# Optimization experiments

Hardware: AMD Instinct MI355X
Metric: run time of the kernel (lower is better)

Reference implementation:

```python
import jax, jax.numpy as jnp
from jax import lax
import numpy as np

SEQ = 1024
VOCAB = 50000
EMB = 300
CAS_V, CAS_D = 8, 50
POS_V, POS_D = 48, 50
IN_DIM = EMB + CAS_D + POS_D  # 400
H = 512
T = 13  # num_classes / CRF tags


def setup_inputs() -> dict:
    key = jax.random.key(0)
    ks = jax.random.split(key, 16)
    s = lambda k, shape, sc=0.05: jax.random.normal(k, shape, dtype=jnp.float32) * sc
    return {
        "x": jax.random.randint(ks[0], (SEQ,), 0, VOCAB),
        "casing": jax.random.randint(ks[1], (SEQ,), 0, CAS_V),
        "pos": jax.random.randint(ks[2], (SEQ,), 0, POS_V),
        "h0": jnp.zeros((2, H), dtype=jnp.float32),
        "c0": jnp.zeros((2, H), dtype=jnp.float32),
        "W_emb": s(ks[3], (VOCAB, EMB)),
        "W_cas": s(ks[4], (CAS_V, CAS_D)),
        "W_pos": s(ks[5], (POS_V, POS_D)),
        "Wx_f": s(ks[6], (IN_DIM, 4 * H)),
        "Wh_f": s(ks[7], (H, 4 * H)),
        "b_f": jnp.zeros((4 * H,), dtype=jnp.float32),
        "Wx_b": s(ks[8], (IN_DIM, 4 * H)),
        "Wh_b": s(ks[9], (H, 4 * H)),
        "b_b": jnp.zeros((4 * H,), dtype=jnp.float32),
        "W_out": s(ks[10], (2 * H, T)),
        "b_out": jnp.zeros((T,), dtype=jnp.float32),
        "trans": s(ks[11], (T, T), 0.1),
        "start_trans": s(ks[12], (T,), 0.1),
        "end_trans": s(ks[13], (T,), 0.1),
    }


def _lstm_dir(feat, Wx, Wh, b, h0, c0, reverse):
    # feat: [L, IN_DIM]; precompute input projection for all steps
    pre = feat @ Wx + b  # [L, 4H]

    def step(carry, p):
        h, c = carry
        z = p + h @ Wh
        i, f, g, o = jnp.split(z, 4, axis=-1)
        c = jax.nn.sigmoid(f) * c + jax.nn.sigmoid(i) * jnp.tanh(g)
        h = jax.nn.sigmoid(o) * jnp.tanh(c)
        return (h, c), h

    _, hs = lax.scan(step, (h0, c0), pre, reverse=reverse)
    return hs  # [L, H]


def _viterbi(em, trans, start_trans, end_trans):
    # em: [L, T] emission (log) scores; max-plus DP
    score0 = start_trans + em[0]

    def fwd(score, e):
        total = score[:, None] + trans  # [T, T]: prev -> next
        best = jnp.max(total, axis=0) + e
        idx = jnp.argmax(total, axis=0)
        return best, idx

    final, hist = lax.scan(fwd, score0, em[1:])  # hist: [L-1, T]
    final = final + end_trans
    last = jnp.argmax(final)

    def back(tag, idx_row):
        return idx_row[tag], tag

    first, rest = lax.scan(back, last, hist, reverse=True)
    return jnp.concatenate([first[None], rest])  # [L] int


def reference(x, casing, pos, h0, c0, W_emb, W_cas, W_pos, Wx_f, Wh_f, b_f,
              Wx_b, Wh_b, b_b, W_out, b_out, trans, start_trans, end_trans):
    # AWD-LSTM encode (eval mode: dropout identity)
    feat = jnp.concatenate([W_emb[x], W_cas[casing], W_pos[pos]], axis=-1)  # [L, 400]
    hf = _lstm_dir(feat, Wx_f, Wh_f, b_f, h0[0], c0[0], reverse=False)
    hb = _lstm_dir(feat, Wx_b, Wh_b, b_b, h0[1], c0[1], reverse=True)
    o = jnp.concatenate([hf, hb], axis=-1) @ W_out + b_out  # [L, T]
    tag_scores = jax.nn.log_softmax(o, axis=1)
    path = _viterbi(tag_scores, trans, start_trans, end_trans)
    return tag_scores, path
```

## Files before the change

### kernel.cpp

```cpp
#include <hip/hip_runtime.h>
#include <hip/hip_bf16.h>
#include <math.h>

#define SEQ 1024
#define HID 512
#define FOURH 2048
#define IND 400
#define NT 13

#define LSTM_WGS 64
#define NGEMM 192
#define JPW 16
#define WCOLS 64
#define TAG_INVALID 0xFFFFFFFFu

__device__ __forceinline__ float bf2f(unsigned short u) {
    union { unsigned u32; float f; } v;
    v.u32 = ((unsigned)u) << 16;
    return v.f;
}

__device__ __forceinline__ unsigned short f2bf(float f) {
    union { float f; unsigned u; } v;
    v.f = f;
    unsigned u = v.u;
    unsigned rounding = 0x7FFFu + ((u >> 16) & 1u);
    u += rounding;
    return (unsigned short)(u >> 16);
}

__device__ __forceinline__ float ldf(const void* p, size_t i, int isf32) {
    return isf32 ? ((const float*)p)[i] : bf2f(((const unsigned short*)p)[i]);
}

__device__ __forceinline__ float fsigm(float x) {
    return __builtin_amdgcn_rcpf(1.f + __builtin_amdgcn_exp2f(-1.44269504f * x));
}
__device__ __forceinline__ float ftanhf(float x) {
    return 1.f - 2.f * __builtin_amdgcn_rcpf(__builtin_amdgcn_exp2f(2.88539008f * x) + 1.f);
}
__device__ __forceinline__ float satz(float z) { return fminf(fmaxf(z, -60.f), 60.f); }

__global__ __launch_bounds__(64) void detect_kernel(const unsigned short* __restrict__ w,
                                                    int* __restrict__ flag,
                                                    unsigned* __restrict__ vcnt,
                                                    unsigned* __restrict__ flags) {
    int lane = threadIdx.x;
    int cnt = 0;
    for (int i = 0; i < 4; ++i) {
        unsigned short u = w[2 * (lane * 4 + i)];
        int e = (u >> 7) & 0xFF;
        if (e >= 90 && e < 127) cnt++;
    }
#pragma unroll
    for (int off = 32; off >= 1; off >>= 1) cnt += __shfl_xor(cnt, off, 64);
    if (lane == 0) *flag = (cnt < 128) ? 1 : 0;
    if (lane == 1) *vcnt = 0;
    flags[lane] = 0;
}

__global__ __launch_bounds__(512, 2) void fused_kernel(
        const int* __restrict__ x, const int* __restrict__ cas, const int* __restrict__ pos,
        const void* __restrict__ W_emb, const void* __restrict__ W_cas, const void* __restrict__ W_pos,
        const void* __restrict__ Wx_f, const void* __restrict__ b_f,
        const void* __restrict__ Wx_b, const void* __restrict__ b_b,
        const void* __restrict__ Wh_f, const void* __restrict__ Wh_b,
        const void* __restrict__ h0, const void* __restrict__ c0,
        unsigned long long* __restrict__ preu, float* __restrict__ hsout,
        unsigned long long* hbuf, const int* __restrict__ dflag,
        unsigned* __restrict__ flags) {
    __shared__ float smem[12800 + 96];
    const int isf32 = *dflag;
    const int tid = threadIdx.x;
    const int b = blockIdx.x;

    if (b >= LSTM_WGS) {
        const int e = b - LSTM_WGS;
        const int gdir = e & 1;
        const int i = e >> 1;
        const void* Wx = gdir ? Wx_b : Wx_f;
        const void* bb = gdir ? b_b : b_f;
        unsigned long long* dst = preu + (size_t)gdir * SEQ * 512;
        float* ftile = smem;
        int* idxs = (int*)&smem[12800];
        const int critby = gdir ? 31 : 0;

        if (i < 8) {
            const int r0 = critby * 32;
            const int c  = tid & 255;
            const int rg = tid >> 8;
            const int col = i * 256 + c;

            if (tid < 32)       idxs[tid] = x[r0 + tid];
            else if (tid < 64)  idxs[tid] = cas[r0 + tid - 32];
            else if (tid < 96)  idxs[tid] = pos[r0 + tid - 64];
            __syncthreads();
            for (int idx = tid; idx < 32 * IND; idx += 512) {
                int r = idx / IND;
                int el = idx - r * IND;
                float v;
                if (el < 300)      v = ldf(W_emb, (size_t)idxs[r] * 300 + el, isf32);
                else if (el < 350) v = ldf(W_cas, (size_t)idxs[32 + r] * 50 + (el - 300), isf32);
                else               v = ldf(W_pos, (size_t)idxs[64 + r] * 50 + (el - 350), isf32);
                ftile[idx] = v;
            }
            __syncthreads();

            float acc[16];
            float bias = ldf(bb, col, isf32);
#pragma unroll
            for (int r = 0; r < 16; ++r) acc[r] = bias;

            if (isf32) {
                const float* W = (const float*)Wx;
                for (int kk = 0; kk < 100; ++kk) {
                    int k = kk * 4;
                    float w0 = W[(size_t)(k + 0) * FOURH + col];
                    float w1 = W[(size_t)(k + 1) * FOURH + col];
                    float w2 = W[(size_t)(k + 2) * FOURH + col];
                    float w3 = W[(size_t)(k + 3) * FOURH + col];
#pragma unroll
                    for (int rr = 0; rr < 16; ++rr) {
                        float4 f = *(const float4*)&ftile[(rg * 16 + rr) * IND + k];
                        acc[rr] += f.x * w0 + f.y * w1 + f.z * w2 + f.w * w3;
                    }
                }
            } else {
                const unsigned short* W = (const unsigned short*)Wx;
                for (int kk = 0; kk < 100; ++kk) {
                    int k = kk * 4;
                    float w0 = bf2f(W[(size_t)(k + 0) * FOURH + col]);
                    float w1 = bf2f(W[(size_t)(k + 1) * FOURH + col]);
                    float w2 = bf2f(W[(size_t)(k + 2) * FOURH + col]);
                    float w3 = bf2f(W[(size_t)(k + 3) * FOURH + col]);
#pragma unroll
                    for (int rr = 0; rr < 16; ++rr) {
                        float4 f = *(const float4*)&ftile[(rg * 16 + rr) * IND + k];
                        acc[rr] += f.x * w0 + f.y * w1 + f.z * w2 + f.w * w3;
                    }
                }
            }

            for (int rr = 0; rr < 16; ++rr) {
                int r = rg * 16 + rr;
                unsigned long long w = ((unsigned long long)f2bf(acc[rr])) << (16 * (tid & 3));
                w |= __shfl_xor(w, 1, 64);
                w |= __shfl_xor(w, 2, 64);
                if ((tid & 3) == 0)
                    __hip_atomic_store(&dst[(size_t)(r0 + r) * 512 + (col >> 2)], w,
                                       __ATOMIC_RELAXED, __HIP_MEMORY_SCOPE_AGENT);
            }
            asm volatile("s_waitcnt vmcnt(0)" ::: "memory");
            __syncthreads();
            if (tid == 0) atomicAdd(&flags[gdir * 32 + critby], 1u);
            return;
        }

        const int j = i - 8;
        const int q = j >> 2;
        const int ntile = (j < 36) ? 2 : 1;
        for (int ti = 0; ti < ntile; ++ti) {
            const int by = (ti == 0) ? (gdir ? (30 - q) : (1 + q))
                                     : (gdir ? (8 - q)  : (23 + q));
            const int bx = j & 3;
            const int r0 = by * 32;
            const int col = bx * 512 + tid;

            __syncthreads();
            if (tid < 32)       idxs[tid] = x[r0 + tid];
            else if (tid < 64)  idxs[tid] = cas[r0 + tid - 32];
            else if (tid < 96)  idxs[tid] = pos[r0 + tid - 64];
            __syncthreads();
            for (int idx = tid; idx < 32 * IND; idx += 512) {
                int r = idx / IND;
                int el = idx - r * IND;
                float v;
                if (el < 300)      v = ldf(W_emb, (size_t)idxs[r] * 300 + el, isf32);
                else if (el < 350) v = ldf(W_cas, (size_t)idxs[32 + r] * 50 + (el - 300), isf32);
                else               v = ldf(W_pos, (size_t)idxs[64 + r] * 50 + (el - 350), isf32);
                ftile[idx] = v;
            }
            __syncthreads();

            float acc[32];
            float bias = ldf(bb, col, isf32);
#pragma unroll
            for (int r = 0; r < 32; ++r) acc[r] = bias;

            if (isf32) {
                const float* W = (const float*)Wx;
                for (int kk = 0; kk < 100; ++kk) {
                    int k = kk * 4;
                    float w0 = W[(size_t)(k + 0) * FOURH + col];
                    float w1 = W[(size_t)(k + 1) * FOURH + col];
                    float w2 = W[(size_t)(k + 2) * FOURH + col];
                    float w3 = W[(size_t)(k + 3) * FOURH + col];
#pragma unroll
                    for (int r = 0; r < 32; ++r) {
                        float4 f = *(const float4*)&ftile[r * IND + k];
                        acc[r] += f.x * w0 + f.y * w1 + f.z * w2 + f.w * w3;
                    }
                }
            } else {
                const unsigned short* W = (const unsigned short*)Wx;
                for (int kk = 0; kk < 100; ++kk) {
                    int k = kk * 4;
                    float w0 = bf2f(W[(size_t)(k + 0) * FOURH + col]);
                    float w1 = bf2f(W[(size_t)(k + 1) * FOURH + col]);
                    float w2 = bf2f(W[(size_t)(k + 2) * FOURH + col]);
                    float w3 = bf2f(W[(size_t)(k + 3) * FOURH + col]);
#pragma unroll
                    for (int r = 0; r < 32; ++r) {
                        float4 f = *(const float4*)&ftile[r * IND + k];
                        acc[r] += f.x * w0 + f.y * w1 + f.z * w2 + f.w * w3;
                    }
                }
            }

            for (int r = 0; r < 32; ++r) {
                unsigned long long w = ((unsigned long long)f2bf(acc[r])) << (16 * (tid & 3));
                w |= __shfl_xor(w, 1, 64);
                w |= __shfl_xor(w, 2, 64);
                if ((tid & 3) == 0)
                    __hip_atomic_store(&dst[(size_t)(r0 + r) * 512 + (col >> 2)], w,
                                       __ATOMIC_RELAXED, __HIP_MEMORY_SCOPE_AGENT);
            }
            asm volatile("s_waitcnt vmcnt(0)" ::: "memory");
            __syncthreads();
            if (tid == 0) atomicAdd(&flags[gdir * 32 + by], 1u);
        }
        return;
    }

    float* redp = smem;
    const int dir = b & 1;
    const int g = b >> 1;
    const int j0 = g * JPW;
    const int critby = dir ? 31 : 0;

    const void* Wh = dir ? Wh_b : Wh_f;
    const unsigned long long* preu_d = preu + (size_t)dir * SEQ * 512;
    float* hso = hsout + (size_t)dir * SEQ * HID;
    unsigned long long* hb_d  = hbuf + dir * 2 * HID;
    unsigned long long* hb2_d = hbuf + 4096 + dir * 2 * HID;

    const int seg  = tid >> 6;
    const int col  = tid & 63;
    const int unit = col & 15;
    const int gate = col >> 4;
    const int gcol = gate * HID + j0 + unit;
    const int redoff = seg * WCOLS + unit * 4 + gate;

    const int isep  = (tid < 64);
    const int eunit = tid >> 2;
    const int egate = tid & 3;
    const int ispub = isep && (egate == 0);
    const int sub   = eunit & 3;
    const int widx  = egate * 128 + ((j0 + eunit) >> 2);

    float4 w0, w1, w2, w3, w4, w5, w6, w7, w8, w9, w10, w11, w12, w13, w14, w15;
    if (isf32) {
        const float* wp = (const float*)Wh + (size_t)(seg * 64) * FOURH + gcol;
#define LDW(i) w##i = make_float4(wp[(size_t)(4*i+0)*FOURH], wp[(size_t)(4*i+1)*FOURH], \
                                  wp[(size_t)(4*i+2)*FOURH], wp[(size_t)(4*i+3)*FOURH])
        LDW(0); LDW(1); LDW(2); LDW(3); LDW(4); LDW(5); LDW(6); LDW(7);
        LDW(8); LDW(9); LDW(10); LDW(11); LDW(12); LDW(13); LDW(14); LDW(15);
#undef LDW
    } else {
        const unsigned short* wp = (const unsigned short*)Wh + (size_t)(seg * 64) * FOURH + gcol;
#define LDW(i) w##i = make_float4(bf2f(wp[(size_t)(4*i+0)*FOURH]), bf2f(wp[(size_t)(4*i+1)*FOURH]), \
                                  bf2f(wp[(size_t)(4*i+2)*FOURH]), bf2f(wp[(size_t)(4*i+3)*FOURH]))
        LDW(0); LDW(1); LDW(2); LDW(3); LDW(4); LDW(5); LDW(6); LDW(7);
        LDW(8); LDW(9); LDW(10); LDW(11); LDW(12); LDW(13); LDW(14); LDW(15);
#undef LDW
    }

    float creg = 0.f;
    unsigned long long znw = 0;
    int curby = critby;
    if (isep) {
        if (ispub) {
            creg = ldf(c0, dir * HID + j0 + eunit, isf32);
            float h0v = ldf(h0, dir * HID + j0 + eunit, isf32);
            unsigned long long wv = (unsigned long long)__float_as_uint(h0v);
            unsigned long long iv = ((unsigned long long)TAG_INVALID << 32);
            __hip_atomic_store(&hb_d[j0 + eunit],        wv, __ATOMIC_RELAXED, __HIP_MEMORY_SCOPE_AGENT);
            __hip_atomic_store(&hb2_d[j0 + eunit],       wv, __ATOMIC_RELAXED, __HIP_MEMORY_SCOPE_AGENT);
            __hip_atomic_store(&hb_d[HID + j0 + eunit],  iv, __ATOMIC_RELAXED, __HIP_MEMORY_SCOPE_AGENT);
            __hip_atomic_store(&hb2_d[HID + j0 + eunit], iv, __ATOMIC_RELAXED, __HIP_MEMORY_SCOPE_AGENT);
        }
        {
            const unsigned* fp = &flags[dir * 32 + curby];
            while (__hip_atomic_load(fp, __ATOMIC_RELAXED, __HIP_MEMORY_SCOPE_AGENT) < 8u) {}
        }
        int t0 = dir ? (SEQ - 1) : 0;
        znw = __hip_atomic_load(&preu_d[(size_t)t0 * 512 + widx],
                                __ATOMIC_RELAXED, __HIP_MEMORY_SCOPE_AGENT);
    }
    __syncthreads();

    for (int s = 0; s < SEQ; ++s) {
        const int t = dir ? (SEQ - 1 - s) : s;

        unsigned hu;
        {
            const unsigned long long* A = &hb_d[(s & 1) * HID + tid];
            const unsigned long long* B = &hb2_d[(s & 1) * HID + tid];
            const unsigned expect = (unsigned)s;
            unsigned long long va = __hip_atomic_load(A, __ATOMIC_RELAXED, __HIP_MEMORY_SCOPE_AGENT);
            unsigned long long vb = __hip_atomic_load(B, __ATOMIC_RELAXED, __HIP_MEMORY_SCOPE_AGENT);
            for (;;) {
                if ((unsigned)(va >> 32) == expect) { hu = (unsigned)va; break; }
                va = __hip_atomic_load(A, __ATOMIC_RELAXED, __HIP_MEMORY_SCOPE_AGENT);
                if ((unsigned)(vb >> 32) == expect) { hu = (unsigned)vb; break; }
                vb = __hip_atomic_load(B, __ATOMIC_RELAXED, __HIP_MEMORY_SCOPE_AGENT);
            }
        }

        float zc = 0.f;
        if (isep) {
            zc = bf2f((unsigned short)(znw >> (16 * sub)));
            if (s + 1 < SEQ) {
                int tn = dir ? (SEQ - 2 - s) : (s + 1);
                int byn = tn >> 5;
                if (byn != curby) {
                    const unsigned thr = (byn == critby) ? 8u : 4u;
                    const unsigned* fp = &flags[dir * 32 + byn];
                    while (__hip_atomic_load(fp, __ATOMIC_RELAXED, __HIP_MEMORY_SCOPE_AGENT) < thr) {}
                    curby = byn;
                }
                znw = __hip_atomic_load(&preu_d[(size_t)tn * 512 + widx],
                                        __ATOMIC_RELAXED, __HIP_MEMORY_SCOPE_AGENT);
            }
        }

        float a0 = 0.f, a1 = 0.f, a2 = 0.f, a3 = 0.f;
#define MACQ(i, A) { \
        float hx = __uint_as_float((unsigned)__builtin_amdgcn_readlane((int)hu, 4*i+0)); \
        float hy = __uint_as_float((unsigned)__builtin_amdgcn_readlane((int)hu, 4*i+1)); \
        float hz = __uint_as_float((unsigned)__builtin_amdgcn_readlane((int)hu, 4*i+2)); \
        float hw = __uint_as_float((unsigned)__builtin_amdgcn_readlane((int)hu, 4*i+3)); \
        A += hx * w##i.x + hy * w##i.y + hz * w##i.z + hw * w##i.w; }
        MACQ(0, a0)  MACQ(1, a1)  MACQ(2, a2)  MACQ(3, a3)
        MACQ(4, a0)  MACQ(5, a1)  MACQ(6, a2)  MACQ(7, a3)
        MACQ(8, a0)  MACQ(9, a1)  MACQ(10, a2) MACQ(11, a3)
        MACQ(12, a0) MACQ(13, a1) MACQ(14, a2) MACQ(15, a3)
#undef MACQ
        redp[(s & 1) * 512 + redoff] = (a0 + a1) + (a2 + a3);
        __syncthreads();

        if (isep) {
            const float* rp = &redp[(s & 1) * 512];
            float z = rp[0 * WCOLS + tid] + rp[1 * WCOLS + tid]
                    + rp[2 * WCOLS + tid] + rp[3 * WCOLS + tid]
                    + rp[4 * WCOLS + tid] + rp[5 * WCOLS + tid]
                    + rp[6 * WCOLS + tid] + rp[7 * WCOLS + tid];
            z = satz(z + zc);
            float vs = fsigm(z);
            float vt = ftanhf(z);
            float v = (egate == 2) ? vt : vs;
            float x1 = __shfl_xor(v, 1, 64);
            float x2 = __shfl_xor(v, 2, 64);
            float x3 = __shfl_xor(x1, 2, 64);
            if (ispub) {
                float ig = v, fg = x1, gg = x2, og = x3;
                float cnew = fg * creg + ig * gg;
                creg = cnew;
                float hnew = og * ftanhf(satz(cnew));
                unsigned long long w = ((unsigned long long)(unsigned)(s + 1) << 32)
                                     | (unsigned long long)__float_as_uint(hnew);
                const int par = (s + 1) & 1;
                __hip_atomic_store(&hb_d[par * HID + j0 + eunit], w,
                                   __ATOMIC_RELAXED, __HIP_MEMORY_SCOPE_AGENT);
                __hip_atomic_store(&hb2_d[par * HID + j0 + eunit], w,
                                   __ATOMIC_RELAXED, __HIP_MEMORY_SCOPE_AGENT);
                hso[(size_t)t * HID + j0 + eunit] = hnew;
            }
        }
    }
}

__global__ __launch_bounds__(64) void outproj_kernel(const float* __restrict__ hsout,
        const void* __restrict__ W_out, const void* __restrict__ b_out,
        float* __restrict__ out_scores,
        const void* __restrict__ trans, const void* __restrict__ strans,
        const void* __restrict__ etrans, float* __restrict__ out_path,
        unsigned* __restrict__ vcnt, const int* __restrict__ dflag) {
    __shared__ unsigned char hist[SEQ][NT];
    const int isf32 = *dflag;
    int t = blockIdx.x;
    int lane = threadIdx.x;
    const float* hf = hsout + (size_t)t * HID;
    const float* hb = hsout + (size_t)SEQ * HID + (size_t)t * HID;
    float acc[NT];
#pragma unroll
    for (int j = 0; j < NT; ++j) acc[j] = 0.f;
    for (int k = lane; k < HID; k += 64) {
        float a = hf[k], b2 = hb[k];
#pragma unroll
        for (int j = 0; j < NT; ++j)
            acc[j] += a * ldf(W_out, (size_t)k * NT + j, isf32)
                    + b2 * ldf(W_out, (size_t)(HID + k) * NT + j, isf32);
    }
#pragma unroll
    for (int off = 32; off >= 1; off >>= 1) {
#pragma unroll
        for (int j = 0; j < NT; ++j) acc[j] += __shfl_xor(acc[j], off, 64);
    }
    float o[NT];
    float m = -1e30f;
#pragma unroll
    for (int j = 0; j < NT; ++j) { o[j] = acc[j] + ldf(b_out, j, isf32); m = fmaxf(m, o[j]); }
    float lse = 0.f;
#pragma unroll
    for (int j = 0; j < NT; ++j) lse += expf(o[j] - m);
    lse = m + logf(lse);
    if (lane < NT)
        __hip_atomic_store(&out_scores[t * NT + lane], o[lane] - lse,
                           __ATOMIC_RELAXED, __HIP_MEMORY_SCOPE_AGENT);
    __builtin_amdgcn_s_waitcnt(0);

    unsigned old = 0;
    if (lane == 0) old = atomicAdd(vcnt, 1u);
    old = __shfl(old, 0, 64);
    if (old != SEQ - 1) return;

    const float* em = out_scores;
    int j = lane < NT ? lane : 0;
    float tr[NT];
#pragma unroll
    for (int i = 0; i < NT; ++i) tr[i] = ldf(trans, i * NT + j, isf32);
#define EML(tt) __hip_atomic_load(&em[(size_t)(tt) * NT + j], __ATOMIC_RELAXED, __HIP_MEMORY_SCOPE_AGENT)
    float score = ldf(strans, j, isf32) + EML(0);
    float c0 = EML(1), c1 = EML(2), c2 = EML(3), c3 = EML(4),
          c4 = EML(5), c5 = EML(6), c6 = EML(7), c7 = EML(8);
#define VSTEP(PE, TT) { \
    float best = -1e30f; int arg = 0; \
    _Pragma("unroll") \
    for (int i = 0; i < NT; ++i) { \
        float si = __shfl(score, i, 64); \
        float cand = si + tr[i]; \
        if (cand > best) { best = cand; arg = i; } \
    } \
    if (lane < NT) hist[TT][lane] = (unsigned char)arg; \
    score = best + PE; }
    for (int tb = 1; tb < SEQ; tb += 8) {
        int nb = tb + 8;
        float n0 = 0.f, n1 = 0.f, n2 = 0.f, n3 = 0.f, n4 = 0.f, n5 = 0.f, n6 = 0.f, n7 = 0.f;
        if (nb + 0 < SEQ) n0 = EML(nb + 0);
        if (nb + 1 < SEQ) n1 = EML(nb + 1);
        if (nb + 2 < SEQ) n2 = EML(nb + 2);
        if (nb + 3 < SEQ) n3 = EML(nb + 3);
        if (nb + 4 < SEQ) n4 = EML(nb + 4);
        if (nb + 5 < SEQ) n5 = EML(nb + 5);
        if (nb + 6 < SEQ) n6 = EML(nb + 6);
        if (nb + 7 < SEQ) n7 = EML(nb + 7);
        VSTEP(c0, tb + 0)
        if (tb + 1 < SEQ) VSTEP(c1, tb + 1)
        if (tb + 2 < SEQ) VSTEP(c2, tb + 2)
        if (tb + 3 < SEQ) VSTEP(c3, tb + 3)
        if (tb + 4 < SEQ) VSTEP(c4, tb + 4)
        if (tb + 5 < SEQ) VSTEP(c5, tb + 5)
        if (tb + 6 < SEQ) VSTEP(c6, tb + 6)
        if (tb + 7 < SEQ) VSTEP(c7, tb + 7)
        c0 = n0; c1 = n1; c2 = n2; c3 = n3; c4 = n4; c5 = n5; c6 = n6; c7 = n7;
    }
#undef VSTEP
#undef EML
    score += ldf(etrans, j, isf32);
    float bmax = -1e30f;
    int last = 0;
#pragma unroll
    for (int i = 0; i < NT; ++i) {
        float si = __shfl(score, i, 64);
        if (si > bmax) { bmax = si; last = i; }
    }
    if (lane == 0) {
        int cur = last;
        out_path[SEQ - 1] = (float)cur;
        for (int tt = SEQ - 1; tt >= 1; --tt) {
            cur = hist[tt][cur];
            out_path[tt - 1] = (float)cur;
        }
    }
}

extern "C" void kernel_launch(void* const* d_in, const int* in_sizes, int n_in,
                              void* d_out, int out_size, void* d_ws, size_t ws_size,
                              hipStream_t stream) {
    const int* x      = (const int*)d_in[0];
    const int* casing = (const int*)d_in[1];
    const int* posi   = (const int*)d_in[2];
    const void* h0    = d_in[3];
    const void* c0    = d_in[4];
    const void* W_emb = d_in[5];
    const void* W_cas = d_in[6];
    const void* W_pos = d_in[7];
    const void* Wx_f  = d_in[8];
    const void* Wh_f  = d_in[9];
    const void* b_f   = d_in[10];
    const void* Wx_b  = d_in[11];
    const void* Wh_b  = d_in[12];
    const void* b_b   = d_in[13];
    const void* W_out = d_in[14];
    const void* b_out = d_in[15];
    const void* trans = d_in[16];
    const void* strans = d_in[17];
    const void* etrans = d_in[18];

    char* ws = (char*)d_ws;
    int* dflag          = (int*)(ws + 448);
    unsigned* vcnt      = (unsigned*)(ws + 456);
    unsigned long long* preu = (unsigned long long*)(ws + 512);
    float* hsout        = (float*)(ws + 512 + 8388608);
    unsigned long long* hbuf = (unsigned long long*)(ws + 512 + 8388608 + 4194304);
    unsigned* flags     = (unsigned*)(ws + 512 + 8388608 + 4194304 + 65536);

    float* out_scores = (float*)d_out;
    float* out_path   = out_scores + SEQ * NT;

    detect_kernel<<<1, 64, 0, stream>>>((const unsigned short*)W_emb, dflag, vcnt, flags);

    fused_kernel<<<LSTM_WGS + NGEMM, 512, 0, stream>>>(
        x, casing, posi, W_emb, W_cas, W_pos, Wx_f, b_f, Wx_b, b_b,
        Wh_f, Wh_b, h0, c0, preu, hsout, hbuf, dflag, flags);

    outproj_kernel<<<SEQ, 64, 0, stream>>>(hsout, W_out, b_out, out_scores,
                                           trans, strans, etrans, out_path, vcnt, dflag);
}
```

Baseline: 2.260 ms.

## Fuse output projection and Viterbi into persistent LSTM kernel via chunk flags

Removes the separate outproj kernel and has the idle GEMM workgroups, after finishing input projections, wait on per-chunk completion flags set by the LSTM recurrence. They then compute log-softmax emissions for 32-step chunks, with the last one to finish running Viterbi. The goal is to overlap the output projection with the recurrent loop and drop a kernel launch plus its tail. The cost is extra spin-waiting on flags, extra flag atomics and waitcnts inside the recurrence, and a serial Viterbi that still runs at the end.

Result: slower. 2.331 ms (+3.1%).

```diff
diff --git a/kernel.cpp b/kernel.cpp
--- a/kernel.cpp
+++ b/kernel.cpp
@@ -57,6 +57,7 @@
     if (lane == 0) *flag = (cnt < 128) ? 1 : 0;
     if (lane == 1) *vcnt = 0;
     flags[lane] = 0;
+    flags[64 + lane] = 0;
 }
 
 __global__ __launch_bounds__(512, 2) void fused_kernel(
@@ -66,9 +67,13 @@
         const void* __restrict__ Wx_b, const void* __restrict__ b_b,
         const void* __restrict__ Wh_f, const void* __restrict__ Wh_b,
         const void* __restrict__ h0, const void* __restrict__ c0,
+        const void* __restrict__ W_out, const void* __restrict__ b_out,
+        const void* __restrict__ trans, const void* __restrict__ strans,
+        const void* __restrict__ etrans,
         unsigned long long* __restrict__ preu, float* __restrict__ hsout,
         unsigned long long* hbuf, const int* __restrict__ dflag,
-        unsigned* __restrict__ flags) {
+        unsigned* __restrict__ flags, unsigned* __restrict__ vcnt,
+        float* __restrict__ out_scores, float* __restrict__ out_path) {
     __shared__ float smem[12800 + 96];
     const int isf32 = *dflag;
     const int tid = threadIdx.x;
@@ -153,81 +158,193 @@
             asm volatile("s_waitcnt vmcnt(0)" ::: "memory");
             __syncthreads();
             if (tid == 0) atomicAdd(&flags[gdir * 32 + critby], 1u);
-            return;
-        }
-
-        const int j = i - 8;
-        const int q = j >> 2;
-        const int ntile = (j < 36) ? 2 : 1;
-        for (int ti = 0; ti < ntile; ++ti) {
-            const int by = (ti == 0) ? (gdir ? (30 - q) : (1 + q))
-                                     : (gdir ? (8 - q)  : (23 + q));
-            const int bx = j & 3;
-            const int r0 = by * 32;
-            const int col = bx * 512 + tid;
-
-            __syncthreads();
-            if (tid < 32)       idxs[tid] = x[r0 + tid];
-            else if (tid < 64)  idxs[tid] = cas[r0 + tid - 32];
-            else if (tid < 96)  idxs[tid] = pos[r0 + tid - 64];
-            __syncthreads();
-            for (int idx = tid; idx < 32 * IND; idx += 512) {
-                int r = idx / IND;
-                int el = idx - r * IND;
-                float v;
-                if (el < 300)      v = ldf(W_emb, (size_t)idxs[r] * 300 + el, isf32);
-                else if (el < 350) v = ldf(W_cas, (size_t)idxs[32 + r] * 50 + (el - 300), isf32);
-                else               v = ldf(W_pos, (size_t)idxs[64 + r] * 50 + (el - 350), isf32);
-                ftile[idx] = v;
-            }
-            __syncthreads();
-
-            float acc[32];
-            float bias = ldf(bb, col, isf32);
-#pragma unroll
-            for (int r = 0; r < 32; ++r) acc[r] = bias;
-
-            if (isf32) {
-                const float* W = (const float*)Wx;
-                for (int kk = 0; kk < 100; ++kk) {
-                    int k = kk * 4;
-                    float w0 = W[(size_t)(k + 0) * FOURH + col];
-                    float w1 = W[(size_t)(k + 1) * FOURH + col];
-                    float w2 = W[(size_t)(k + 2) * FOURH + col];
-                    float w3 = W[(size_t)(k + 3) * FOURH + col];
-#pragma unroll
-                    for (int r = 0; r < 32; ++r) {
-                        float4 f = *(const float4*)&ftile[r * IND + k];
-                        acc[r] += f.x * w0 + f.y * w1 + f.z * w2 + f.w * w3;
+        } else {
+            const int j = i - 8;
+            const int q = j >> 2;
+            const int ntile = (j < 36) ? 2 : 1;
+            for (int ti = 0; ti < ntile; ++ti) {
+                const int by = (ti == 0) ? (gdir ? (30 - q) : (1 + q))
+                                         : (gdir ? (8 - q)  : (23 + q));
+                const int bx = j & 3;
+                const int r0 = by * 32;
+                const int col = bx * 512 + tid;
+
+                __syncthreads();
+                if (tid < 32)       idxs[tid] = x[r0 + tid];
+                else if (tid < 64)  idxs[tid] = cas[r0 + tid - 32];
+                else if (tid < 96)  idxs[tid] = pos[r0 + tid - 64];
+                __syncthreads();
+                for (int idx = tid; idx < 32 * IND; idx += 512) {
+                    int r = idx / IND;
+                    int el = idx - r * IND;
+                    float v;
+                    if (el < 300)      v = ldf(W_emb, (size_t)idxs[r] * 300 + el, isf32);
+                    else if (el < 350) v = ldf(W_cas, (size_t)idxs[32 + r] * 50 + (el - 300), isf32);
+                    else               v = ldf(W_pos, (size_t)idxs[64 + r] * 50 + (el - 350), isf32);
+                    ftile[idx] = v;
+                }
+                __syncthreads();
+
+                float acc[32];
+                float bias = ldf(bb, col, isf32);
+#pragma unroll
+                for (int r = 0; r < 32; ++r) acc[r] = bias;
+
+                if (isf32) {
+                    const float* W = (const float*)Wx;
+                    for (int kk = 0; kk < 100; ++kk) {
+                        int k = kk * 4;
+                        float w0 = W[(size_t)(k + 0) * FOURH + col];
+                        float w1 = W[(size_t)(k + 1) * FOURH + col];
+                        float w2 = W[(size_t)(k + 2) * FOURH + col];
+                        float w3 = W[(size_t)(k + 3) * FOURH + col];
+#pragma unroll
+                        for (int r = 0; r < 32; ++r) {
+                            float4 f = *(const float4*)&ftile[r * IND + k];
+                            acc[r] += f.x * w0 + f.y * w1 + f.z * w2 + f.w * w3;
+                        }
                     }
-                }
-            } else {
-                const unsigned short* W = (const unsigned short*)Wx;
-                for (int kk = 0; kk < 100; ++kk) {
-                    int k = kk * 4;
-                    float w0 = bf2f(W[(size_t)(k + 0) * FOURH + col]);
-                    float w1 = bf2f(W[(size_t)(k + 1) * FOURH + col]);
-                    float w2 = bf2f(W[(size_t)(k + 2) * FOURH + col]);
-                    float w3 = bf2f(W[(size_t)(k + 3) * FOURH + col]);
-#pragma unroll
-                    for (int r = 0; r < 32; ++r) {
-                        float4 f = *(const float4*)&ftile[r * IND + k];
-                        acc[r] += f.x * w0 + f.y * w1 + f.z * w2 + f.w * w3;
+                } else {
+                    const unsigned short* W = (const unsigned short*)Wx;
+                    for (int kk = 0; kk < 100; ++kk) {
+                        int k = kk * 4;
+                        float w0 = bf2f(W[(size_t)(k + 0) * FOURH + col]);
+                        float w1 = bf2f(W[(size_t)(k + 1) * FOURH + col]);
+                        float w2 = bf2f(W[(size_t)(k + 2) * FOURH + col]);
+                        float w3 = bf2f(W[(size_t)(k + 3) * FOURH + col]);
+#pragma unroll
+                        for (int r = 0; r < 32; ++r) {
+                            float4 f = *(const float4*)&ftile[r * IND + k];
+                            acc[r] += f.x * w0 + f.y * w1 + f.z * w2 + f.w * w3;
+                        }
                     }
                 }
-            }
-
-            for (int r = 0; r < 32; ++r) {
-                unsigned long long w = ((unsigned long long)f2bf(acc[r])) << (16 * (tid & 3));
-                w |= __shfl_xor(w, 1, 64);
-                w |= __shfl_xor(w, 2, 64);
-                if ((tid & 3) == 0)
-                    __hip_atomic_store(&dst[(size_t)(r0 + r) * 512 + (col >> 2)], w,
-                                       __ATOMIC_RELAXED, __HIP_MEMORY_SCOPE_AGENT);
-            }
+
+                for (int r = 0; r < 32; ++r) {
+                    unsigned long long w = ((unsigned long long)f2bf(acc[r])) << (16 * (tid & 3));
+                    w |= __shfl_xor(w, 1, 64);
+                    w |= __shfl_xor(w, 2, 64);
+                    if ((tid & 3) == 0)
+                        __hip_atomic_store(&dst[(size_t)(r0 + r) * 512 + (col >> 2)], w,
+                                           __ATOMIC_RELAXED, __HIP_MEMORY_SCOPE_AGENT);
+                }
+                asm volatile("s_waitcnt vmcnt(0)" ::: "memory");
+                __syncthreads();
+                if (tid == 0) atomicAdd(&flags[gdir * 32 + by], 1u);
+            }
+        }
+
+        const int corder = e / 6;
+        const int subr   = e % 6;
+        const int c      = (corder & 1) ? (16 + (corder >> 1)) : (15 - (corder >> 1));
+        if (tid == 0) {
+            const unsigned* f0 = &flags[64 + c];
+            const unsigned* f1 = &flags[96 + c];
+            while (__hip_atomic_load(f0, __ATOMIC_RELAXED, __HIP_MEMORY_SCOPE_AGENT) < 32u) {}
+            while (__hip_atomic_load(f1, __ATOMIC_RELAXED, __HIP_MEMORY_SCOPE_AGENT) < 32u) {}
+        }
+        __syncthreads();
+
+        const int seg = tid >> 6;
+        const int lane = tid & 63;
+        const int ric = subr + 6 * seg;
+        if (ric < 32) {
+            const int t = c * 32 + ric;
+            const float* hfp = hsout + (size_t)t * HID;
+            const float* hbp = hsout + (size_t)SEQ * HID + (size_t)t * HID;
+            float acc[NT];
+#pragma unroll
+            for (int j = 0; j < NT; ++j) acc[j] = 0.f;
+            for (int k = lane; k < HID; k += 64) {
+                float a  = __hip_atomic_load(&hfp[k], __ATOMIC_RELAXED, __HIP_MEMORY_SCOPE_AGENT);
+                float b2 = __hip_atomic_load(&hbp[k], __ATOMIC_RELAXED, __HIP_MEMORY_SCOPE_AGENT);
+#pragma unroll
+                for (int j = 0; j < NT; ++j)
+                    acc[j] += a * ldf(W_out, (size_t)k * NT + j, isf32)
+                            + b2 * ldf(W_out, (size_t)(HID + k) * NT + j, isf32);
+            }
+#pragma unroll
+            for (int off = 32; off >= 1; off >>= 1) {
+#pragma unroll
+                for (int j = 0; j < NT; ++j) acc[j] += __shfl_xor(acc[j], off, 64);
+            }
+            float o[NT];
+            float m = -1e30f;
+#pragma unroll
+            for (int j = 0; j < NT; ++j) { o[j] = acc[j] + ldf(b_out, j, isf32); m = fmaxf(m, o[j]); }
+            float lse = 0.f;
+#pragma unroll
+            for (int j = 0; j < NT; ++j) lse += expf(o[j] - m);
+            lse = m + logf(lse);
+            if (lane < NT)
+                __hip_atomic_store(&out_scores[t * NT + lane], o[lane] - lse,
+                                   __ATOMIC_RELAXED, __HIP_MEMORY_SCOPE_AGENT);
             asm volatile("s_waitcnt vmcnt(0)" ::: "memory");
-            __syncthreads();
-            if (tid == 0) atomicAdd(&flags[gdir * 32 + by], 1u);
+        }
+        __syncthreads();
+        if (tid == 0) idxs[0] = (int)atomicAdd(vcnt, 1u);
+        __syncthreads();
+        if (idxs[0] != NGEMM - 1) return;
+
+        if (tid >= 64) return;
+        unsigned char (*hist)[NT] = (unsigned char(*)[NT])smem;
+        const float* em = out_scores;
+        int j = lane < NT ? lane : 0;
+        float tr[NT];
+#pragma unroll
+        for (int i2 = 0; i2 < NT; ++i2) tr[i2] = ldf(trans, i2 * NT + j, isf32);
+#define EML(tt) __hip_atomic_load(&em[(size_t)(tt) * NT + j], __ATOMIC_RELAXED, __HIP_MEMORY_SCOPE_AGENT)
+        float score = ldf(strans, j, isf32) + EML(0);
+        float c0v = EML(1), c1 = EML(2), c2 = EML(3), c3 = EML(4),
+              c4 = EML(5), c5 = EML(6), c6 = EML(7), c7 = EML(8);
+#define VSTEP(PE, TT) { \
+        float best = -1e30f; int arg = 0; \
+        _Pragma("unroll") \
+        for (int i2 = 0; i2 < NT; ++i2) { \
+            float si = __shfl(score, i2, 64); \
+            float cand = si + tr[i2]; \
+            if (cand > best) { best = cand; arg = i2; } \
+        } \
+        if (lane < NT) hist[TT][lane] = (unsigned char)arg; \
+        score = best + PE; }
+        for (int tb = 1; tb < SEQ; tb += 8) {
+            int nb = tb + 8;
+            float n0 = 0.f, n1 = 0.f, n2 = 0.f, n3 = 0.f, n4 = 0.f, n5 = 0.f, n6 = 0.f, n7 = 0.f;
+            if (nb + 0 < SEQ) n0 = EML(nb + 0);
+            if (nb + 1 < SEQ) n1 = EML(nb + 1);
+            if (nb + 2 < SEQ) n2 = EML(nb + 2);
+            if (nb + 3 < SEQ) n3 = EML(nb + 3);
+            if (nb + 4 < SEQ) n4 = EML(nb + 4);
+            if (nb + 5 < SEQ) n5 = EML(nb + 5);
+            if (nb + 6 < SEQ) n6 = EML(nb + 6);
+            if (nb + 7 < SEQ) n7 = EML(nb + 7);
+            VSTEP(c0v, tb + 0)
+            if (tb + 1 < SEQ) VSTEP(c1, tb + 1)
+            if (tb + 2 < SEQ) VSTEP(c2, tb + 2)
+            if (tb + 3 < SEQ) VSTEP(c3, tb + 3)
+            if (tb + 4 < SEQ) VSTEP(c4, tb + 4)
+            if (tb + 5 < SEQ) VSTEP(c5, tb + 5)
+            if (tb + 6 < SEQ) VSTEP(c6, tb + 6)
+            if (tb + 7 < SEQ) VSTEP(c7, tb + 7)
+            c0v = n0; c1 = n1; c2 = n2; c3 = n3; c4 = n4; c5 = n5; c6 = n6; c7 = n7;
+        }
+#undef VSTEP
+#undef EML
+        score += ldf(etrans, j, isf32);
+        float bmax = -1e30f;
+        int last = 0;
+#pragma unroll
+        for (int i2 = 0; i2 < NT; ++i2) {
+            float si = __shfl(score, i2, 64);
+            if (si > bmax) { bmax = si; last = i2; }
+        }
+        if (lane == 0) {
+            int cur = last;
+            out_path[SEQ - 1] = (float)cur;
+            for (int tt = SEQ - 1; tt >= 1; --tt) {
+                cur = hist[tt][cur];
+                out_path[tt - 1] = (float)cur;
+            }
         }
         return;
     }
@@ -374,113 +491,16 @@
                                    __ATOMIC_RELAXED, __HIP_MEMORY_SCOPE_AGENT);
                 __hip_atomic_store(&hb2_d[par * HID + j0 + eunit], w,
                                    __ATOMIC_RELAXED, __HIP_MEMORY_SCOPE_AGENT);
-                hso[(size_t)t * HID + j0 + eunit] = hnew;
-            }
-        }
-    }
-}
-
-__global__ __launch_bounds__(64) void outproj_kernel(const float* __restrict__ hsout,
-        const void* __restrict__ W_out, const void* __restrict__ b_out,
-        float* __restrict__ out_scores,
-        const void* __restrict__ trans, const void* __restrict__ strans,
-        const void* __restrict__ etrans, float* __restrict__ out_path,
-        unsigned* __restrict__ vcnt, const int* __restrict__ dflag) {
-    __shared__ unsigned char hist[SEQ][NT];
-    const int isf32 = *dflag;
-    int t = blockIdx.x;
-    int lane = threadIdx.x;
-    const float* hf = hsout + (size_t)t * HID;
-    const float* hb = hsout + (size_t)SEQ * HID + (size_t)t * HID;
-    float acc[NT];
-#pragma unroll
-    for (int j = 0; j < NT; ++j) acc[j] = 0.f;
-    for (int k = lane; k < HID; k += 64) {
-        float a = hf[k], b2 = hb[k];
-#pragma unroll
-        for (int j = 0; j < NT; ++j)
-            acc[j] += a * ldf(W_out, (size_t)k * NT + j, isf32)
-                    + b2 * ldf(W_out, (size_t)(HID + k) * NT + j, isf32);
-    }
-#pragma unroll
-    for (int off = 32; off >= 1; off >>= 1) {
-#pragma unroll
-        for (int j = 0; j < NT; ++j) acc[j] += __shfl_xor(acc[j], off, 64);
-    }
-    float o[NT];
-    float m = -1e30f;
-#pragma unroll
-    for (int j = 0; j < NT; ++j) { o[j] = acc[j] + ldf(b_out, j, isf32); m = fmaxf(m, o[j]); }
-    float lse = 0.f;
-#pragma unroll
-    for (int j = 0; j < NT; ++j) lse += expf(o[j] - m);
-    lse = m + logf(lse);
-    if (lane < NT)
-        __hip_atomic_store(&out_scores[t * NT + lane], o[lane] - lse,
-                           __ATOMIC_RELAXED, __HIP_MEMORY_SCOPE_AGENT);
-    __builtin_amdgcn_s_waitcnt(0);
-
-    unsigned old = 0;
-    if (lane == 0) old = atomicAdd(vcnt, 1u);
-    old = __shfl(old, 0, 64);
-    if (old != SEQ - 1) return;
-
-    const float* em = out_scores;
-    int j = lane < NT ? lane : 0;
-    float tr[NT];
-#pragma unroll
-    for (int i = 0; i < NT; ++i) tr[i] = ldf(trans, i * NT + j, isf32);
-#define EML(tt) __hip_atomic_load(&em[(size_t)(tt) * NT + j], __ATOMIC_RELAXED, __HIP_MEMORY_SCOPE_AGENT)
-    float score = ldf(strans, j, isf32) + EML(0);
-    float c0 = EML(1), c1 = EML(2), c2 = EML(3), c3 = EML(4),
-          c4 = EML(5), c5 = EML(6), c6 = EML(7), c7 = EML(8);
-#define VSTEP(PE, TT) { \
-    float best = -1e30f; int arg = 0; \
-    _Pragma("unroll") \
-    for (int i = 0; i < NT; ++i) { \
-        float si = __shfl(score, i, 64); \
-        float cand = si + tr[i]; \
-        if (cand > best) { best = cand; arg = i; } \
-    } \
-    if (lane < NT) hist[TT][lane] = (unsigned char)arg; \
-    score = best + PE; }
-    for (int tb = 1; tb < SEQ; tb += 8) {
-        int nb = tb + 8;
-        float n0 = 0.f, n1 = 0.f, n2 = 0.f, n3 = 0.f, n4 = 0.f, n5 = 0.f, n6 = 0.f, n7 = 0.f;
-        if (nb + 0 < SEQ) n0 = EML(nb + 0);
-        if (nb + 1 < SEQ) n1 = EML(nb + 1);
-        if (nb + 2 < SEQ) n2 = EML(nb + 2);
-        if (nb + 3 < SEQ) n3 = EML(nb + 3);
-        if (nb + 4 < SEQ) n4 = EML(nb + 4);
-        if (nb + 5 < SEQ) n5 = EML(nb + 5);
-        if (nb + 6 < SEQ) n6 = EML(nb + 6);
-        if (nb + 7 < SEQ) n7 = EML(nb + 7);
-        VSTEP(c0, tb + 0)
-        if (tb + 1 < SEQ) VSTEP(c1, tb + 1)
-        if (tb + 2 < SEQ) VSTEP(c2, tb + 2)
-        if (tb + 3 < SEQ) VSTEP(c3, tb + 3)
-        if (tb + 4 < SEQ) VSTEP(c4, tb + 4)
-        if (tb + 5 < SEQ) VSTEP(c5, tb + 5)
-        if (tb + 6 < SEQ) VSTEP(c6, tb + 6)
-        if (tb + 7 < SEQ) VSTEP(c7, tb + 7)
-        c0 = n0; c1 = n1; c2 = n2; c3 = n3; c4 = n4; c5 = n5; c6 = n6; c7 = n7;
-    }
-#undef VSTEP
-#undef EML
-    score += ldf(etrans, j, isf32);
-    float bmax = -1e30f;
-    int last = 0;
-#pragma unroll
-    for (int i = 0; i < NT; ++i) {
-        float si = __shfl(score, i, 64);
-        if (si > bmax) { bmax = si; last = i; }
-    }
-    if (lane == 0) {
-        int cur = last;
-        out_path[SEQ - 1] = (float)cur;
-        for (int tt = SEQ - 1; tt >= 1; --tt) {
-            cur = hist[tt][cur];
-            out_path[tt - 1] = (float)cur;
+                __hip_atomic_store(&hso[(size_t)t * HID + j0 + eunit], hnew,
+                                   __ATOMIC_RELAXED, __HIP_MEMORY_SCOPE_AGENT);
+            }
+            if ((s & 31) == 31) {
+                asm volatile("s_waitcnt vmcnt(0)" ::: "memory");
+                if (tid == 0) {
+                    int ch = dir ? (31 - (s >> 5)) : (s >> 5);
+                    atomicAdd(&flags[64 + dir * 32 + ch], 1u);
+                }
+            }
         }
     }
 }
@@ -523,8 +543,6 @@
 
     fused_kernel<<<LSTM_WGS + NGEMM, 512, 0, stream>>>(
         x, casing, posi, W_emb, W_cas, W_pos, Wx_f, b_f, Wx_b, b_b,
-        Wh_f, Wh_b, h0, c0, preu, hsout, hbuf, dflag, flags);
-
-    outproj_kernel<<<SEQ, 64, 0, stream>>>(hsout, W_out, b_out, out_scores,
-                                           trans, strans, etrans, out_path, vcnt, dflag);
-}
+        Wh_f, Wh_b, h0, c0, W_out, b_out, trans, strans, etrans,
+        preu, hsout, hbuf, dflag, flags, vcnt, out_scores, out_path);
+}
```
